# Kernel tuning notes

Measured on AMD Instinct MI355X. Metric: run time of the kernel, lower is better.

The kernel has to match this reference:

```python
import jax, jax.numpy as jnp
import numpy as np

N_NODES = 50000
N_EDGES = 800000
D_FEAT = 64
HIDDEN = 128
OUT = 16


def sage_conv(x, src, dst, W_l, W_r, b):
    # PyG SAGEConv (aggr='mean', root_weight=True):
    #   out = lin_l(mean_{j in N(i)} x_j) + lin_r(x_i)
    n = x.shape[0]
    msg = x[src]                                        # [E, d] gather
    agg = jax.ops.segment_sum(msg, dst, num_segments=n) # [N, d]
    deg = jax.ops.segment_sum(jnp.ones((src.shape[0],), x.dtype), dst, num_segments=n)
    mean = agg / jnp.maximum(deg, 1.0)[:, None]         # 0 for isolated nodes
    return mean @ W_l + b + x @ W_r


def setup_inputs() -> dict:
    key = jax.random.key(0)
    ks = jax.random.split(key, 8)
    s = lambda d: 1.0 / np.sqrt(d)
    return {
        "x": jax.random.normal(ks[0], (N_NODES, D_FEAT), dtype=jnp.float32),
        "edge_index": jax.random.randint(ks[1], (2, N_EDGES), 0, N_NODES, dtype=jnp.int32),
        "W1_l": jax.random.normal(ks[2], (D_FEAT, HIDDEN), dtype=jnp.float32) * s(D_FEAT),
        "W1_r": jax.random.normal(ks[3], (D_FEAT, HIDDEN), dtype=jnp.float32) * s(D_FEAT),
        "b1": jnp.zeros((HIDDEN,), dtype=jnp.float32),
        "W2_l": jax.random.normal(ks[4], (HIDDEN, OUT), dtype=jnp.float32) * s(HIDDEN),
        "W2_r": jax.random.normal(ks[5], (HIDDEN, OUT), dtype=jnp.float32) * s(HIDDEN),
        "b2": jnp.zeros((OUT,), dtype=jnp.float32),
    }


def reference(x, edge_index, W1_l, W1_r, b1, W2_l, W2_r, b2):
    src, dst = edge_index[0], edge_index[1]
    h = jax.nn.relu(sage_conv(x, src, dst, W1_l, W1_r, b1))
    h = sage_conv(h, src, dst, W2_l, W2_r, b2)
    # eval-mode path of the original module
    return jax.nn.softmax(h, axis=1)
```

## Files before the change

### kernel.cpp

```cpp
#include <hip/hip_runtime.h>
#include <math.h>

#define N_NODES 50000
#define N_EDGES 800000
#define D_FEAT  64
#define HIDDEN  128
#define OUT     16
#define CAP     64
#define NXCD    8
#define DPG     (N_NODES / NXCD)

typedef unsigned short ushort_t;
typedef unsigned int uint_t;
typedef __attribute__((ext_vector_type(8))) __bf16 bf16x8;
typedef __attribute__((ext_vector_type(4))) float f32x4;

__device__ __forceinline__ float4 fma4(float s, float4 w, float4 a) {
    a.x += s * w.x; a.y += s * w.y; a.z += s * w.z; a.w += s * w.w;
    return a;
}

#define SPLIT8(AH, AL, U0, U1) { \
    float v_; __bf16 h_; \
    v_ = U0.x; h_ = (__bf16)v_; AH[0] = h_; AL[0] = (__bf16)(v_ - (float)h_); \
    v_ = U0.y; h_ = (__bf16)v_; AH[1] = h_; AL[1] = (__bf16)(v_ - (float)h_); \
    v_ = U0.z; h_ = (__bf16)v_; AH[2] = h_; AL[2] = (__bf16)(v_ - (float)h_); \
    v_ = U0.w; h_ = (__bf16)v_; AH[3] = h_; AL[3] = (__bf16)(v_ - (float)h_); \
    v_ = U1.x; h_ = (__bf16)v_; AH[4] = h_; AL[4] = (__bf16)(v_ - (float)h_); \
    v_ = U1.y; h_ = (__bf16)v_; AH[5] = h_; AL[5] = (__bf16)(v_ - (float)h_); \
    v_ = U1.z; h_ = (__bf16)v_; AH[6] = h_; AL[6] = (__bf16)(v_ - (float)h_); \
    v_ = U1.w; h_ = (__bf16)v_; AH[7] = h_; AL[7] = (__bf16)(v_ - (float)h_); \
}

__global__ __launch_bounds__(256) void wprep_kernel(
        const float* __restrict__ W1l, const float* __restrict__ W1r,
        const float* __restrict__ W2l, const float* __restrict__ W2r,
        const int* __restrict__ ei,
        __bf16* __restrict__ Whi1, __bf16* __restrict__ Wlo1,
        __bf16* __restrict__ Whi2, __bf16* __restrict__ Wlo2,
        uint_t* __restrict__ ep,
        int* __restrict__ cnt) {
    const int idx = blockIdx.x * 256 + threadIdx.x;
    for (int i = idx; i < N_NODES; i += 800 * 256) cnt[i] = 0;
    if (idx < N_EDGES / 4) {
        const int e4 = idx * 4;
        const int4 s = *(const int4*)(ei + e4);
        const int4 d = *(const int4*)(ei + N_EDGES + e4);
        uint4 p;
        p.x = (uint_t)s.x | ((uint_t)d.x << 16);
        p.y = (uint_t)s.y | ((uint_t)d.y << 16);
        p.z = (uint_t)s.z | ((uint_t)d.z << 16);
        p.w = (uint_t)s.w | ((uint_t)d.w << 16);
        *(uint4*)(ep + e4) = p;
    }
    if (idx < 16384) {
        const int k = idx >> 7, c = idx & 127;
        const float v = (k < 64) ? W1l[k * HIDDEN + c] : W1r[(k - 64) * HIDDEN + c];
        const int kt = k >> 5, g = (k >> 3) & 3, j = k & 7;
        const int pos = (((kt * 8 + (c >> 4)) * 64) + (g * 16 + (c & 15))) * 8 + j;
        const __bf16 h = (__bf16)v;
        Whi1[pos] = h;
        Wlo1[pos] = (__bf16)(v - (float)h);
    } else if (idx < 20480) {
        const int i2 = idx - 16384;
        const int k = i2 >> 5, c = i2 & 31;
        const float v = (c < 16) ? W2l[k * OUT + c] : W2r[k * OUT + (c - 16)];
        const int kt = k >> 5, g = (k >> 3) & 3, j = k & 7;
        const int pos = (((kt * 2 + (c >> 4)) * 64) + (g * 16 + (c & 15))) * 8 + j;
        const __bf16 h = (__bf16)v;
        Whi2[pos] = h;
        Wlo2[pos] = (__bf16)(v - (float)h);
    }
}

__global__ __launch_bounds__(256) void adjfill_kernel(
        const uint_t* __restrict__ ep,
        int* __restrict__ cnt,
        ushort_t* __restrict__ adj) {
    const int g = blockIdx.x & (NXCD - 1);
    const int b = blockIdx.x >> 3;
    const int e4 = (b * 256 + threadIdx.x) * 4;
    if (e4 >= N_EDGES) return;
    const uint4 v = *(const uint4*)(ep + e4);
    const uint_t lo = (uint_t)(g * DPG), hi = lo + DPG;
#define PUT(U) { \
        const uint_t d_ = (U) >> 16; \
        if (d_ >= lo && d_ < hi) { \
            int p = atomicAdd(&cnt[d_], 1); \
            if (p < CAP) adj[d_ * CAP + p] = (ushort_t)((U) & 0xFFFFu); \
        } }
    PUT(v.x) PUT(v.y) PUT(v.z) PUT(v.w)
#undef PUT
}

__global__ __launch_bounds__(256) void gather_mean_kernel(
        const float* __restrict__ x,
        const ushort_t* __restrict__ adj,
        const int* __restrict__ cnt,
        float* __restrict__ mean) {
    const int w = (blockIdx.x * 256 + threadIdx.x) >> 6;
    if (w >= N_NODES) return;
    const int lane = threadIdx.x & 63;
    const int eg = lane >> 4, fq = lane & 15;
    int deg = cnt[w];
    if (deg > CAP) deg = CAP;
    const int start = w * CAP;
    float4 acc = {0.f, 0.f, 0.f, 0.f};
    int j = eg;
    for (; j + 4 < deg; j += 8) {
        const int s0 = adj[start + j], s1 = adj[start + j + 4];
        const float4 v0 = *(const float4*)(x + s0 * D_FEAT + 4 * fq);
        const float4 v1 = *(const float4*)(x + s1 * D_FEAT + 4 * fq);
        acc.x += v0.x + v1.x; acc.y += v0.y + v1.y;
        acc.z += v0.z + v1.z; acc.w += v0.w + v1.w;
    }
    if (j < deg) {
        const int s0 = adj[start + j];
        const float4 v0 = *(const float4*)(x + s0 * D_FEAT + 4 * fq);
        acc.x += v0.x; acc.y += v0.y; acc.z += v0.z; acc.w += v0.w;
    }
    acc.x += __shfl_down(acc.x, 32); acc.y += __shfl_down(acc.y, 32);
    acc.z += __shfl_down(acc.z, 32); acc.w += __shfl_down(acc.w, 32);
    acc.x += __shfl_down(acc.x, 16); acc.y += __shfl_down(acc.y, 16);
    acc.z += __shfl_down(acc.z, 16); acc.w += __shfl_down(acc.w, 16);
    if (lane < 16) {
        const float invd = 1.f / fmaxf((float)deg, 1.f);
        float4 o;
        o.x = acc.x * invd; o.y = acc.y * invd;
        o.z = acc.z * invd; o.w = acc.w * invd;
        *(float4*)(mean + w * D_FEAT + 4 * fq) = o;
    }
}

__global__ __launch_bounds__(256) void mfma1_kernel(
        const float* __restrict__ x,
        const float* __restrict__ mean,
        const __bf16* __restrict__ Whi1, const __bf16* __restrict__ Wlo1,
        const __bf16* __restrict__ Whi2, const __bf16* __restrict__ Wlo2,
        const float* __restrict__ b1,
        float* __restrict__ z, float* __restrict__ rbuf) {
    __shared__ float Hs[4][16][132];
    const int w = threadIdx.x >> 6;
    const int l = threadIdx.x & 63;
    const int g = l >> 4;
    const int col = l & 15;
    const int nodebase = blockIdx.x * 64 + w * 16;
    const int nA = nodebase + col;

    f32x4 acc[8];
    #pragma unroll
    for (int ct = 0; ct < 8; ++ct) acc[ct] = (f32x4){0.f, 0.f, 0.f, 0.f};

    #pragma unroll
    for (int kt = 0; kt < 4; ++kt) {
        float4 u0 = {0.f, 0.f, 0.f, 0.f}, u1 = {0.f, 0.f, 0.f, 0.f};
        if (nA < N_NODES) {
            const float* p = ((kt < 2) ? mean : x)
                             + (size_t)nA * 64 + (kt & 1) * 32 + g * 8;
            u0 = *(const float4*)p;
            u1 = *(const float4*)(p + 4);
        }
        bf16x8 ah, al;
        SPLIT8(ah, al, u0, u1)
        #pragma unroll
        for (int ct = 0; ct < 8; ++ct) {
            const int fo = ((kt * 8 + ct) * 64 + l) * 8;
            const bf16x8 bh = *(const bf16x8*)(Whi1 + fo);
            const bf16x8 bl = *(const bf16x8*)(Wlo1 + fo);
            acc[ct] = __builtin_amdgcn_mfma_f32_16x16x32_bf16(ah, bh, acc[ct], 0, 0, 0);
            acc[ct] = __builtin_amdgcn_mfma_f32_16x16x32_bf16(al, bh, acc[ct], 0, 0, 0);
            acc[ct] = __builtin_amdgcn_mfma_f32_16x16x32_bf16(ah, bl, acc[ct], 0, 0, 0);
        }
    }

    #pragma unroll
    for (int ct = 0; ct < 8; ++ct) {
        const float bv = b1[ct * 16 + col];
        #pragma unroll
        for (int i = 0; i < 4; ++i)
            Hs[w][g * 4 + i][ct * 16 + col] = fmaxf(acc[ct][i] + bv, 0.f);
    }

    f32x4 acc2[2];
    acc2[0] = (f32x4){0.f, 0.f, 0.f, 0.f};
    acc2[1] = (f32x4){0.f, 0.f, 0.f, 0.f};
    #pragma unroll
    for (int kt2 = 0; kt2 < 4; ++kt2) {
        const float* hp = &Hs[w][col][kt2 * 32 + g * 8];
        const float4 u0 = *(const float4*)hp;
        const float4 u1 = *(const float4*)(hp + 4);
        bf16x8 ah, al;
        SPLIT8(ah, al, u0, u1)
        #pragma unroll
        for (int ct2 = 0; ct2 < 2; ++ct2) {
            const int fo = ((kt2 * 2 + ct2) * 64 + l) * 8;
            const bf16x8 bh = *(const bf16x8*)(Whi2 + fo);
            const bf16x8 bl = *(const bf16x8*)(Wlo2 + fo);
            acc2[ct2] = __builtin_amdgcn_mfma_f32_16x16x32_bf16(ah, bh, acc2[ct2], 0, 0, 0);
            acc2[ct2] = __builtin_amdgcn_mfma_f32_16x16x32_bf16(al, bh, acc2[ct2], 0, 0, 0);
            acc2[ct2] = __builtin_amdgcn_mfma_f32_16x16x32_bf16(ah, bl, acc2[ct2], 0, 0, 0);
        }
    }
    #pragma unroll
    for (int ct2 = 0; ct2 < 2; ++ct2) {
        float* dst = ct2 ? rbuf : z;
        #pragma unroll
        for (int i = 0; i < 4; ++i) {
            const int node = nodebase + g * 4 + i;
            if (node < N_NODES) dst[node * OUT + col] = acc2[ct2][i];
        }
    }
}

__global__ __launch_bounds__(256) void fused2_kernel(
        const float* __restrict__ z,
        const float* __restrict__ r_in,
        const ushort_t* __restrict__ adj,
        const int* __restrict__ cnt,
        const float* __restrict__ b2,
        float* __restrict__ out) {
    const int w = (blockIdx.x * 256 + threadIdx.x) >> 6;
    if (w >= N_NODES) return;
    const int lane = threadIdx.x & 63;
    const int eg = lane >> 2, kq = lane & 3;
    int deg = cnt[w];
    if (deg > CAP) deg = CAP;
    const int start = w * CAP;
    float4 acc = {0.f, 0.f, 0.f, 0.f};
    for (int j = eg; j < deg; j += 16) {
        const float4 v = *(const float4*)(z + adj[start + j] * OUT + 4 * kq);
        acc.x += v.x; acc.y += v.y; acc.z += v.z; acc.w += v.w;
    }
    #pragma unroll
    for (int off = 32; off >= 4; off >>= 1) {
        acc.x += __shfl_down(acc.x, off); acc.y += __shfl_down(acc.y, off);
        acc.z += __shfl_down(acc.z, off); acc.w += __shfl_down(acc.w, off);
    }
    const float invd = 1.f / fmaxf((float)deg, 1.f);
    const float4 rv = *(const float4*)(r_in + w * OUT + 4 * (lane & 3));
    const float4 bv = *(const float4*)(b2 + 4 * (lane & 3));
    float4 s;
    s.x = acc.x * invd + rv.x + bv.x;
    s.y = acc.y * invd + rv.y + bv.y;
    s.z = acc.z * invd + rv.z + bv.z;
    s.w = acc.w * invd + rv.w + bv.w;
    float m = fmaxf(fmaxf(s.x, s.y), fmaxf(s.z, s.w));
    m = fmaxf(m, __shfl_xor(m, 1));
    m = fmaxf(m, __shfl_xor(m, 2));
    float4 e;
    e.x = __expf(s.x - m); e.y = __expf(s.y - m);
    e.z = __expf(s.z - m); e.w = __expf(s.w - m);
    float t = e.x + e.y + e.z + e.w;
    t += __shfl_xor(t, 1);
    t += __shfl_xor(t, 2);
    if (lane < 4) {
        const float it = 1.f / t;
        float4 o;
        o.x = e.x * it; o.y = e.y * it; o.z = e.z * it; o.w = e.w * it;
        *(float4*)(out + w * OUT + 4 * lane) = o;
    }
}

extern "C" void kernel_launch(void* const* d_in, const int* in_sizes, int n_in,
                              void* d_out, int out_size, void* d_ws, size_t ws_size,
                              hipStream_t stream) {
    const float* x   = (const float*)d_in[0];
    const int*   ei  = (const int*)d_in[1];
    const float* W1l = (const float*)d_in[2];
    const float* W1r = (const float*)d_in[3];
    const float* b1  = (const float*)d_in[4];
    const float* W2l = (const float*)d_in[5];
    const float* W2r = (const float*)d_in[6];
    const float* b2  = (const float*)d_in[7];
    float* out = (float*)d_out;

    char* wsB = (char*)d_ws;
    int*      cnt  = (int*)wsB;
    ushort_t* adj  = (ushort_t*)(wsB + 200000);
    float*    mean = (float*)(wsB + 6600000);
    float*    z    = (float*)(wsB + 19400000);
    float*    rbuf = (float*)(wsB + 22600000);
    __bf16*   Whi1 = (__bf16*)(wsB + 25800000);
    __bf16*   Wlo1 = Whi1 + 16384;
    __bf16*   Whi2 = Wlo1 + 16384;
    __bf16*   Wlo2 = Whi2 + 4096;
    uint_t*   ep   = (uint_t*)(wsB + 25881920);

    wprep_kernel<<<800, 256, 0, stream>>>(W1l, W1r, W2l, W2r, ei,
                                          Whi1, Wlo1, Whi2, Wlo2, ep, cnt);
    {
        const int bpg = (N_EDGES / 4 + 255) / 256;
        adjfill_kernel<<<bpg * NXCD, 256, 0, stream>>>(ep, cnt, adj);
    }
    gather_mean_kernel<<<N_NODES / 4, 256, 0, stream>>>(x, adj, cnt, mean);
    mfma1_kernel<<<(N_NODES + 63) / 64, 256, 0, stream>>>(
        x, mean, Whi1, Wlo1, Whi2, Wlo2, b1, z, rbuf);
    fused2_kernel<<<N_NODES / 4, 256, 0, stream>>>(z, rbuf, adj, cnt, b2, out);
}
```

Measured before the change: 113.8 us.

## Store x and mean in fp16, pad degree counters, and compact the workspace

```diff
diff --git a/kernel.cpp b/kernel.cpp
--- a/kernel.cpp
+++ b/kernel.cpp
@@ -9,39 +9,37 @@
 #define CAP     64
 #define NXCD    8
 #define DPG     (N_NODES / NXCD)
+#define CSTR    32
 
 typedef unsigned short ushort_t;
 typedef unsigned int uint_t;
 typedef __attribute__((ext_vector_type(8))) __bf16 bf16x8;
+typedef __attribute__((ext_vector_type(8))) _Float16 half8;
 typedef __attribute__((ext_vector_type(4))) float f32x4;
 
-__device__ __forceinline__ float4 fma4(float s, float4 w, float4 a) {
-    a.x += s * w.x; a.y += s * w.y; a.z += s * w.z; a.w += s * w.w;
-    return a;
-}
-
-#define SPLIT8(AH, AL, U0, U1) { \
-    float v_; __bf16 h_; \
-    v_ = U0.x; h_ = (__bf16)v_; AH[0] = h_; AL[0] = (__bf16)(v_ - (float)h_); \
-    v_ = U0.y; h_ = (__bf16)v_; AH[1] = h_; AL[1] = (__bf16)(v_ - (float)h_); \
-    v_ = U0.z; h_ = (__bf16)v_; AH[2] = h_; AL[2] = (__bf16)(v_ - (float)h_); \
-    v_ = U0.w; h_ = (__bf16)v_; AH[3] = h_; AL[3] = (__bf16)(v_ - (float)h_); \
-    v_ = U1.x; h_ = (__bf16)v_; AH[4] = h_; AL[4] = (__bf16)(v_ - (float)h_); \
-    v_ = U1.y; h_ = (__bf16)v_; AH[5] = h_; AL[5] = (__bf16)(v_ - (float)h_); \
-    v_ = U1.z; h_ = (__bf16)v_; AH[6] = h_; AL[6] = (__bf16)(v_ - (float)h_); \
-    v_ = U1.w; h_ = (__bf16)v_; AH[7] = h_; AL[7] = (__bf16)(v_ - (float)h_); \
+__device__ __forceinline__ void split8(const float* u, bf16x8& ah, bf16x8& al) {
+    #pragma unroll
+    for (int i = 0; i < 8; ++i) {
+        const __bf16 h = (__bf16)u[i];
+        ah[i] = h;
+        al[i] = (__bf16)(u[i] - (float)h);
+    }
 }
 
 __global__ __launch_bounds__(256) void wprep_kernel(
         const float* __restrict__ W1l, const float* __restrict__ W1r,
         const float* __restrict__ W2l, const float* __restrict__ W2r,
-        const int* __restrict__ ei,
+        const int* __restrict__ ei, const float* __restrict__ x,
         __bf16* __restrict__ Whi1, __bf16* __restrict__ Wlo1,
         __bf16* __restrict__ Whi2, __bf16* __restrict__ Wlo2,
-        uint_t* __restrict__ ep,
+        uint_t* __restrict__ ep, _Float16* __restrict__ xh,
         int* __restrict__ cnt) {
     const int idx = blockIdx.x * 256 + threadIdx.x;
-    for (int i = idx; i < N_NODES; i += 800 * 256) cnt[i] = 0;
+    {
+        const int4 z4 = {0, 0, 0, 0};
+        for (int i = idx; i < N_NODES * CSTR / 4; i += 800 * 256)
+            ((int4*)cnt)[i] = z4;
+    }
     if (idx < N_EDGES / 4) {
         const int e4 = idx * 4;
         const int4 s = *(const int4*)(ei + e4);
@@ -52,6 +50,17 @@
         p.z = (uint_t)s.z | ((uint_t)d.z << 16);
         p.w = (uint_t)s.w | ((uint_t)d.w << 16);
         *(uint4*)(ep + e4) = p;
+    }
+    if (idx < N_NODES * D_FEAT / 16) {
+        const float4* xp = (const float4*)(x + idx * 16);
+        const float4 a = xp[0], b = xp[1], c = xp[2], d = xp[3];
+        half8 h0, h1;
+        h0[0] = (_Float16)a.x; h0[1] = (_Float16)a.y; h0[2] = (_Float16)a.z; h0[3] = (_Float16)a.w;
+        h0[4] = (_Float16)b.x; h0[5] = (_Float16)b.y; h0[6] = (_Float16)b.z; h0[7] = (_Float16)b.w;
+        h1[0] = (_Float16)c.x; h1[1] = (_Float16)c.y; h1[2] = (_Float16)c.z; h1[3] = (_Float16)c.w;
+        h1[4] = (_Float16)d.x; h1[5] = (_Float16)d.y; h1[6] = (_Float16)d.z; h1[7] = (_Float16)d.w;
+        *(half8*)(xh + idx * 16) = h0;
+        *(half8*)(xh + idx * 16 + 8) = h1;
     }
     if (idx < 16384) {
         const int k = idx >> 7, c = idx & 127;
@@ -86,7 +95,7 @@
 #define PUT(U) { \
         const uint_t d_ = (U) >> 16; \
         if (d_ >= lo && d_ < hi) { \
-            int p = atomicAdd(&cnt[d_], 1); \
+            int p = atomicAdd(&cnt[d_ * CSTR], 1); \
             if (p < CAP) adj[d_ * CAP + p] = (ushort_t)((U) & 0xFFFFu); \
         } }
     PUT(v.x) PUT(v.y) PUT(v.z) PUT(v.w)
@@ -94,47 +103,51 @@
 }
 
 __global__ __launch_bounds__(256) void gather_mean_kernel(
-        const float* __restrict__ x,
+        const _Float16* __restrict__ xh,
         const ushort_t* __restrict__ adj,
         const int* __restrict__ cnt,
-        float* __restrict__ mean) {
+        _Float16* __restrict__ meanh) {
     const int w = (blockIdx.x * 256 + threadIdx.x) >> 6;
     if (w >= N_NODES) return;
     const int lane = threadIdx.x & 63;
-    const int eg = lane >> 4, fq = lane & 15;
-    int deg = cnt[w];
+    const int eg = lane >> 3, fq = lane & 7;
+    int deg = cnt[w * CSTR];
     if (deg > CAP) deg = CAP;
     const int start = w * CAP;
-    float4 acc = {0.f, 0.f, 0.f, 0.f};
+    float acc[8];
+    #pragma unroll
+    for (int i = 0; i < 8; ++i) acc[i] = 0.f;
     int j = eg;
-    for (; j + 4 < deg; j += 8) {
-        const int s0 = adj[start + j], s1 = adj[start + j + 4];
-        const float4 v0 = *(const float4*)(x + s0 * D_FEAT + 4 * fq);
-        const float4 v1 = *(const float4*)(x + s1 * D_FEAT + 4 * fq);
-        acc.x += v0.x + v1.x; acc.y += v0.y + v1.y;
-        acc.z += v0.z + v1.z; acc.w += v0.w + v1.w;
+    for (; j + 8 < deg; j += 16) {
+        const int s0 = adj[start + j], s1 = adj[start + j + 8];
+        const half8 v0 = *(const half8*)(xh + s0 * D_FEAT + 8 * fq);
+        const half8 v1 = *(const half8*)(xh + s1 * D_FEAT + 8 * fq);
+        #pragma unroll
+        for (int i = 0; i < 8; ++i) acc[i] += (float)v0[i] + (float)v1[i];
     }
     if (j < deg) {
         const int s0 = adj[start + j];
-        const float4 v0 = *(const float4*)(x + s0 * D_FEAT + 4 * fq);
-        acc.x += v0.x; acc.y += v0.y; acc.z += v0.z; acc.w += v0.w;
-    }
-    acc.x += __shfl_down(acc.x, 32); acc.y += __shfl_down(acc.y, 32);
-    acc.z += __shfl_down(acc.z, 32); acc.w += __shfl_down(acc.w, 32);
-    acc.x += __shfl_down(acc.x, 16); acc.y += __shfl_down(acc.y, 16);
-    acc.z += __shfl_down(acc.z, 16); acc.w += __shfl_down(acc.w, 16);
-    if (lane < 16) {
+        const half8 v0 = *(const half8*)(xh + s0 * D_FEAT + 8 * fq);
+        #pragma unroll
+        for (int i = 0; i < 8; ++i) acc[i] += (float)v0[i];
+    }
+    #pragma unroll
+    for (int off = 32; off >= 8; off >>= 1) {
+        #pragma unroll
+        for (int i = 0; i < 8; ++i) acc[i] += __shfl_down(acc[i], off);
+    }
+    if (lane < 8) {
         const float invd = 1.f / fmaxf((float)deg, 1.f);
-        float4 o;
-        o.x = acc.x * invd; o.y = acc.y * invd;
-        o.z = acc.z * invd; o.w = acc.w * invd;
-        *(float4*)(mean + w * D_FEAT + 4 * fq) = o;
+        half8 o;
+        #pragma unroll
+        for (int i = 0; i < 8; ++i) o[i] = (_Float16)(acc[i] * invd);
+        *(half8*)(meanh + w * D_FEAT + 8 * fq) = o;
     }
 }
 
 __global__ __launch_bounds__(256) void mfma1_kernel(
         const float* __restrict__ x,
-        const float* __restrict__ mean,
+        const _Float16* __restrict__ meanh,
         const __bf16* __restrict__ Whi1, const __bf16* __restrict__ Wlo1,
         const __bf16* __restrict__ Whi2, const __bf16* __restrict__ Wlo2,
         const float* __restrict__ b1,
@@ -153,15 +166,24 @@
 
     #pragma unroll
     for (int kt = 0; kt < 4; ++kt) {
-        float4 u0 = {0.f, 0.f, 0.f, 0.f}, u1 = {0.f, 0.f, 0.f, 0.f};
+        float u[8];
+        #pragma unroll
+        for (int i = 0; i < 8; ++i) u[i] = 0.f;
         if (nA < N_NODES) {
-            const float* p = ((kt < 2) ? mean : x)
-                             + (size_t)nA * 64 + (kt & 1) * 32 + g * 8;
-            u0 = *(const float4*)p;
-            u1 = *(const float4*)(p + 4);
+            if (kt < 2) {
+                const half8 hv = *(const half8*)(meanh + (size_t)nA * 64 + kt * 32 + g * 8);
+                #pragma unroll
+                for (int i = 0; i < 8; ++i) u[i] = (float)hv[i];
+            } else {
+                const float* p = x + (size_t)nA * 64 + (kt & 1) * 32 + g * 8;
+                const float4 u0 = *(const float4*)p;
+                const float4 u1 = *(const float4*)(p + 4);
+                u[0] = u0.x; u[1] = u0.y; u[2] = u0.z; u[3] = u0.w;
+                u[4] = u1.x; u[5] = u1.y; u[6] = u1.z; u[7] = u1.w;
+            }
         }
         bf16x8 ah, al;
-        SPLIT8(ah, al, u0, u1)
+        split8(u, ah, al);
         #pragma unroll
         for (int ct = 0; ct < 8; ++ct) {
             const int fo = ((kt * 8 + ct) * 64 + l) * 8;
@@ -189,8 +211,11 @@
         const float* hp = &Hs[w][col][kt2 * 32 + g * 8];
         const float4 u0 = *(const float4*)hp;
         const float4 u1 = *(const float4*)(hp + 4);
+        float u[8];
+        u[0] = u0.x; u[1] = u0.y; u[2] = u0.z; u[3] = u0.w;
+        u[4] = u1.x; u[5] = u1.y; u[6] = u1.z; u[7] = u1.w;
         bf16x8 ah, al;
-        SPLIT8(ah, al, u0, u1)
+        split8(u, ah, al);
         #pragma unroll
         for (int ct2 = 0; ct2 < 2; ++ct2) {
             const int fo = ((kt2 * 2 + ct2) * 64 + l) * 8;
@@ -223,7 +248,7 @@
     if (w >= N_NODES) return;
     const int lane = threadIdx.x & 63;
     const int eg = lane >> 2, kq = lane & 3;
-    int deg = cnt[w];
+    int deg = cnt[w * CSTR];
     if (deg > CAP) deg = CAP;
     const int start = w * CAP;
     float4 acc = {0.f, 0.f, 0.f, 0.f};
@@ -275,25 +300,26 @@
     float* out = (float*)d_out;
 
     char* wsB = (char*)d_ws;
-    int*      cnt  = (int*)wsB;
-    ushort_t* adj  = (ushort_t*)(wsB + 200000);
-    float*    mean = (float*)(wsB + 6600000);
-    float*    z    = (float*)(wsB + 19400000);
-    float*    rbuf = (float*)(wsB + 22600000);
-    __bf16*   Whi1 = (__bf16*)(wsB + 25800000);
-    __bf16*   Wlo1 = Whi1 + 16384;
-    __bf16*   Whi2 = Wlo1 + 16384;
-    __bf16*   Wlo2 = Whi2 + 4096;
-    uint_t*   ep   = (uint_t*)(wsB + 25881920);
-
-    wprep_kernel<<<800, 256, 0, stream>>>(W1l, W1r, W2l, W2r, ei,
-                                          Whi1, Wlo1, Whi2, Wlo2, ep, cnt);
+    int*       cnt   = (int*)wsB;
+    ushort_t*  adj   = (ushort_t*)(wsB + 6400000);
+    uint_t*    ep    = (uint_t*)(wsB + 12800000);
+    float*     z     = (float*)(wsB + 12800000);
+    _Float16*  xh    = (_Float16*)(wsB + 16000000);
+    float*     rbuf  = (float*)(wsB + 16000000);
+    _Float16*  meanh = (_Float16*)(wsB + 22400000);
+    __bf16*    Whi1  = (__bf16*)(wsB + 28800000);
+    __bf16*    Wlo1  = Whi1 + 16384;
+    __bf16*    Whi2  = Wlo1 + 16384;
+    __bf16*    Wlo2  = Whi2 + 4096;
+
+    wprep_kernel<<<800, 256, 0, stream>>>(W1l, W1r, W2l, W2r, ei, x,
+                                          Whi1, Wlo1, Whi2, Wlo2, ep, xh, cnt);
     {
         const int bpg = (N_EDGES / 4 + 255) / 256;
         adjfill_kernel<<<bpg * NXCD, 256, 0, stream>>>(ep, cnt, adj);
     }
-    gather_mean_kernel<<<N_NODES / 4, 256, 0, stream>>>(x, adj, cnt, mean);
+    gather_mean_kernel<<<N_NODES / 4, 256, 0, stream>>>(xh, adj, cnt, meanh);
     mfma1_kernel<<<(N_NODES + 63) / 64, 256, 0, stream>>>(
-        x, mean, Whi1, Wlo1, Whi2, Wlo2, b1, z, rbuf);
+        x, meanh, Whi1, Wlo1, Whi2, Wlo2, b1, z, rbuf);
     fused2_kernel<<<N_NODES / 4, 256, 0, stream>>>(z, rbuf, adj, cnt, b2, out);
 }
```

Result: faster. 105.1 us (-7.6%).
